# Kernel tuning notes

Hardware: AMD Instinct MI355X
Metric: run time of the kernel (lower is better)

Reference implementation:

```python
import jax, jax.numpy as jnp
import numpy as np

B, H, W, K = 4, 512, 512, 64
LAMBDA_SEP = 300.0
LAMBDA_MEAN = 300.0


def _huber(d):
    # torch.nn.functional.huber_loss elementwise, delta=1.0
    a = jnp.abs(d)
    return jnp.where(a < 1.0, 0.5 * a * a, a - 0.5)


def setup_inputs() -> dict:
    key = jax.random.key(0)
    k1, k2 = jax.random.split(key)
    prediction = jax.random.normal(k1, (B, 3, H, W), jnp.float32) * 2.0
    # integer instance labels in [0, K); force every instance to appear
    labels = jax.random.randint(k2, (B, H, W), 0, K)
    labels = labels.at[:, 0, :K].set(jnp.arange(K))
    # palette: instance k -> RGB (0, 0, k); id 0 is background (0,0,0)
    target = jnp.zeros((B, 3, H, W), jnp.float32).at[:, 2].set(labels.astype(jnp.float32))
    no_bg = jnp.ones((B,), bool)
    dist_weights = jnp.ones((K, K), jnp.float32)  # distances=None -> all weights 1.0
    palette_ids = jnp.arange(K, dtype=jnp.int32)  # r*65536 + g*256 + b per palette color
    return {"prediction": prediction, "target": target, "no_bg": no_bg,
            "dist_weights": dist_weights, "palette_ids": palette_ids}


def reference(prediction, target, no_bg, dist_weights, palette_ids):
    P = jnp.transpose(prediction, (0, 2, 3, 1)).astype(jnp.float32)  # [B,H,W,3]
    T = jnp.transpose(target, (0, 2, 3, 1))                          # [B,H,W,3]
    Kk = palette_ids.shape[0]
    h, w = P.shape[1], P.shape[2]
    # pixel instance id (exact for small int-valued floats)
    pid = T[..., 0] * 65536.0 + T[..., 1] * 256.0 + T[..., 2]        # [B,H,W]
    masks = (pid[..., None] == palette_ids.astype(pid.dtype)).astype(P.dtype)  # [B,H,W,K]
    counts = masks.sum((1, 2))                                       # [B,K]
    means = jnp.einsum('bhwk,bhwc->bkc', masks, P) / counts[..., None]  # [B,K,3]
    is_bg = palette_ids == 0                                          # [K]
    # bg instance is counted only when no_bg[b] is False
    counted = (~is_bg)[None, :] | (~no_bg)[:, None]                   # [B,K]
    cf = counted.astype(P.dtype)
    # --- intra-instance huber loss (toward instance mean; zeros for bg) ---
    means_z = jnp.where(is_bg[None, :, None], 0.0, means)             # bg target/mean = 0
    mean_pix = jnp.einsum('bhwk,bkc->bhwc', masks, means_z)           # per-pixel target
    hp = _huber(P - mean_pix).sum(-1)                                 # [B,H,W]
    intra_k = jnp.einsum('bhwk,bhw->bk', masks, hp) / (counts * 3.0)  # mean over pix*3
    intra = (intra_k * cf).sum(-1)                                    # [B]
    # --- inter-instance separation (non-bg instances only) ---
    P2 = (P * P).sum(-1)                                              # [B,H,W]
    M2 = (means * means).sum(-1)                                      # [B,K]
    d2 = P2[..., None] + M2[:, None, None, :] - 2.0 * jnp.einsum('bhwc,bkc->bhwk', P, means)
    sep = LAMBDA_SEP / (1.0 + d2)                                     # [B,H,W,K]
    w_pix = jnp.einsum('bhwj,kj->bhwk', masks, dist_weights)          # weight(k, inst(pixel))
    other = 1.0 - masks                                               # pixels not in k
    num = jnp.einsum('bhwk,bhwk,bhwk->bk', sep, w_pix, other)
    n_other = h * w - counts
    inter_k = num / n_other * (10.0 / jnp.sqrt(counts))
    inter = (inter_k * (~is_bg).astype(P.dtype)[None, :]).sum(-1)     # [B]
    # --- mean-level repulsion among counted instance means ---
    diff = means_z[:, :, None, :] - means_z[:, None, :, :]            # [B,K,K,3]
    sqd = (diff * diff).sum(-1)
    pen = dist_weights[None] * LAMBDA_MEAN / (sqd + 1.0)
    triu = jnp.triu(jnp.ones((Kk, Kk), P.dtype), k=1)
    pairmask = cf[:, :, None] * cf[:, None, :] * triu[None]
    npairs = pairmask.sum((1, 2))
    mean_sep = jnp.where(npairs > 0, (pen * pairmask).sum((1, 2)) / jnp.maximum(npairs, 1.0), 0.0)
    ct = jnp.maximum(cf.sum(-1), 1.0)
    loss_b = (intra + inter + mean_sep) / ct
    return jnp.mean(loss_b)
```

## Files before the change

kernel.cpp:

```cpp
#include <hip/hip_runtime.h>

#define KINST 64

typedef float v2f __attribute__((ext_vector_type(2)));

__device__ __forceinline__ int decode_k0(float t0, float t1, float t2,
                                         const int* pal_s) {
  int pid = (int)(fmaf(t0, 65536.f, fmaf(t1, 256.f, t2)) + 0.5f);
  if (pid >= 0 && pid < KINST && pal_s[pid] == pid) return pid;
  for (int j = 0; j < KINST; ++j)
    if (pal_s[j] == pid) return j;
  return KINST;
}

__global__ __launch_bounds__(256) void k_stats(const float* __restrict__ pred,
                                               const float* __restrict__ targ,
                                               const int* __restrict__ pal,
                                               float* __restrict__ partialS,
                                               unsigned char* __restrict__ k0c,
                                               float* __restrict__ out,
                                               int HW) {
  int b = blockIdx.y;
  __shared__ float ls[4][4][KINST];
  __shared__ int pal_s[KINST];
  if (blockIdx.x == 0 && blockIdx.y == 0 && threadIdx.x == 0) out[0] = 0.f;
  for (int i = threadIdx.x; i < 4 * 4 * KINST; i += blockDim.x)
    (&ls[0][0][0])[i] = 0.f;
  for (int i = threadIdx.x; i < KINST; i += blockDim.x) pal_s[i] = pal[i];
  __syncthreads();
  int w = threadIdx.x >> 6;
  const float* tb = targ + (size_t)b * 3 * HW;
  const float* pb = pred + (size_t)b * 3 * HW;
  unsigned char* kb = k0c ? k0c + (size_t)b * HW : nullptr;
  int nq = HW >> 2;
  const float4* tb4 = (const float4*)tb;
  const float4* pb4 = (const float4*)pb;
  for (int q = blockIdx.x * blockDim.x + threadIdx.x; q < nq;
       q += gridDim.x * blockDim.x) {
    float4 t0 = tb4[q], t1 = tb4[q + nq], t2 = tb4[q + 2 * nq];
    float4 p0 = pb4[q], p1 = pb4[q + nq], p2 = pb4[q + 2 * nq];
    int ka = decode_k0(t0.x, t1.x, t2.x, pal_s);
    int kc = decode_k0(t0.y, t1.y, t2.y, pal_s);
    int kd = decode_k0(t0.z, t1.z, t2.z, pal_s);
    int ke = decode_k0(t0.w, t1.w, t2.w, pal_s);
    if (ka < KINST) {
      atomicAdd(&ls[w][0][ka], p0.x); atomicAdd(&ls[w][1][ka], p1.x);
      atomicAdd(&ls[w][2][ka], p2.x); atomicAdd(&ls[w][3][ka], 1.f);
    }
    if (kc < KINST) {
      atomicAdd(&ls[w][0][kc], p0.y); atomicAdd(&ls[w][1][kc], p1.y);
      atomicAdd(&ls[w][2][kc], p2.y); atomicAdd(&ls[w][3][kc], 1.f);
    }
    if (kd < KINST) {
      atomicAdd(&ls[w][0][kd], p0.z); atomicAdd(&ls[w][1][kd], p1.z);
      atomicAdd(&ls[w][2][kd], p2.z); atomicAdd(&ls[w][3][kd], 1.f);
    }
    if (ke < KINST) {
      atomicAdd(&ls[w][0][ke], p0.w); atomicAdd(&ls[w][1][ke], p1.w);
      atomicAdd(&ls[w][2][ke], p2.w); atomicAdd(&ls[w][3][ke], 1.f);
    }
    if (kb) {
      uchar4 kk = make_uchar4((unsigned char)ka, (unsigned char)kc,
                              (unsigned char)kd, (unsigned char)ke);
      *(uchar4*)(kb + 4 * (size_t)q) = kk;
    }
  }
  for (int i = (nq << 2) + blockIdx.x * blockDim.x + threadIdx.x; i < HW;
       i += gridDim.x * blockDim.x) {
    int k0 = decode_k0(tb[i], tb[i + HW], tb[i + 2 * HW], pal_s);
    if (kb) kb[i] = (unsigned char)k0;
    if (k0 < KINST) {
      atomicAdd(&ls[w][0][k0], pb[i]); atomicAdd(&ls[w][1][k0], pb[i + HW]);
      atomicAdd(&ls[w][2][k0], pb[i + 2 * HW]); atomicAdd(&ls[w][3][k0], 1.f);
    }
  }
  __syncthreads();
  float* o = partialS + ((size_t)b * gridDim.x + blockIdx.x) * 256;
  int i = threadIdx.x;
  int c = i >> 6, k = i & 63;
  o[i] = ls[0][c][k] + ls[1][c][k] + ls[2][c][k] + ls[3][c][k];
}

__global__ __launch_bounds__(256) void k_reduce(const float* __restrict__ partialS,
                                                const float* __restrict__ dw,
                                                const int* __restrict__ pal,
                                                const unsigned char* __restrict__ nb_raw,
                                                int ndw, int nbs,
                                                float* __restrict__ sums,
                                                float4* __restrict__ A_g,
                                                float* __restrict__ W_g,
                                                float4* __restrict__ Z_g,
                                                float* __restrict__ cw_g,
                                                int* __restrict__ flagp,
                                                int B, int HW) {
  int b = blockIdx.x;
  int i = threadIdx.x;
  __shared__ float red[256];
  __shared__ float scale_sh[KINST];
  __shared__ int nu_sh;
  const float* src = partialS + (size_t)b * nbs * 256;
  float s0 = 0.f, s1 = 0.f, s2 = 0.f, s3 = 0.f;
  float s4 = 0.f, s5 = 0.f, s6 = 0.f, s7 = 0.f;
  int bx = 0;
  for (; bx + 8 <= nbs; bx += 8) {
    s0 += src[(size_t)(bx + 0) * 256 + i];
    s1 += src[(size_t)(bx + 1) * 256 + i];
    s2 += src[(size_t)(bx + 2) * 256 + i];
    s3 += src[(size_t)(bx + 3) * 256 + i];
    s4 += src[(size_t)(bx + 4) * 256 + i];
    s5 += src[(size_t)(bx + 5) * 256 + i];
    s6 += src[(size_t)(bx + 6) * 256 + i];
    s7 += src[(size_t)(bx + 7) * 256 + i];
  }
  for (; bx < nbs; ++bx) s0 += src[(size_t)bx * 256 + i];
  float acc = ((s0 + s1) + (s2 + s3)) + ((s4 + s5) + (s6 + s7));
  red[i] = acc;
  sums[((size_t)b * KINST + (i & 63)) * 4 + (i >> 6)] = acc;
  if (i == 0) nu_sh = 0;
  __syncthreads();
  {
    int per = (ndw + B - 1) / B;
    int lo = b * per, hi = min(lo + per, ndw);
    float d0 = dw[0];
    int nu = 0;
    for (int x = lo + i; x < hi; x += blockDim.x) nu |= (dw[x] != d0);
    if (nu) atomicOr(&nu_sh, 1);
  }
  __syncthreads();
  if (i < KINST) {
    float m0s = red[i], m1s = red[64 + i], m2s = red[128 + i], cnt = red[192 + i];
    float inv = cnt > 0.f ? 1.f / cnt : 0.f;
    float m0 = m0s * inv, m1 = m1s * inv, m2 = m2s * inv;
    bool isbg = (pal[i] == 0);
    bool nb = (nb_raw[b] != 0) || (nb_raw[4 * b] != 0);
    float cf = (!isbg || !nb) ? 1.f : 0.f;
    float sc = (!isbg && cnt > 0.f) ? 10.f / (((float)HW - cnt) * sqrtf(cnt)) : 0.f;
    A_g[b * 65 + i] = make_float4(-2.f * m0, -2.f * m1, -2.f * m2,
                                  m0 * m0 + m1 * m1 + m2 * m2 + 1.f);
    Z_g[b * 65 + i] = make_float4(isbg ? 0.f : m0, isbg ? 0.f : m1,
                                  isbg ? 0.f : m2,
                                  cnt > 0.f ? cf / (3.f * cnt) : 0.f);
    W_g[b * 65 + i] = 300.f * dw[0] * sc;
    scale_sh[i] = sc;
  }
  if (i == KINST) {
    A_g[b * 65 + KINST] = make_float4(0.f, 0.f, 0.f, 1.f);
    Z_g[b * 65 + KINST] = make_float4(0.f, 0.f, 0.f, 0.f);
    W_g[b * 65 + KINST] = 0.f;
  }
  __syncthreads();
  if (i == 0) flagp[b] = nu_sh;
  if (nu_sh) {
    float* ct = cw_g + (size_t)b * KINST * 65;
    for (int t2 = i; t2 < KINST * 65; t2 += blockDim.x) {
      int kk = t2 / 65, j = t2 - kk * 65;
      float v = 0.f;
      if (j < KINST && j != kk) v = 300.f * dw[kk * KINST + j] * scale_sh[kk];
      ct[t2] = v;
    }
  }
}

template <bool USE_CACHE>
__global__ __launch_bounds__(256) void k_pix(const float* __restrict__ pred,
                                             const float* __restrict__ targ,
                                             const unsigned char* __restrict__ k0c,
                                             const int* __restrict__ pal,
                                             const float4* __restrict__ A_g,
                                             const float* __restrict__ W_g,
                                             const float4* __restrict__ Z_g,
                                             const float* __restrict__ cw_g,
                                             const int* __restrict__ flagp,
                                             float* __restrict__ res_part,
                                             int HW, int B) {
  int b = blockIdx.y;
  __shared__ float4 A_s[KINST + 1];
  __shared__ float4 Z_s[KINST + 1];
  __shared__ float W_s[KINST + 1];
  __shared__ float cwN[KINST][KINST + 1];
  __shared__ int pal_s[KINST];
  __shared__ int nonuni_s;
  __shared__ float rA[4], rB[4];
  int t = threadIdx.x;
  if (t < KINST + 1) {
    A_s[t] = A_g[b * 65 + t];
    Z_s[t] = Z_g[b * 65 + t];
    W_s[t] = W_g[b * 65 + t];
  }
  if (!USE_CACHE && t < KINST) pal_s[t] = pal[t];
  if (t == 0) {
    int f = 0;
    for (int bb = 0; bb < B; ++bb) f |= flagp[bb];
    nonuni_s = f;
  }
  __syncthreads();
  bool nonuni = nonuni_s != 0;
  if (nonuni) {
    const float* cwb = cw_g + (size_t)b * KINST * 65;
    for (int i = t; i < KINST * 65; i += blockDim.x) (&cwN[0][0])[i] = cwb[i];
    __syncthreads();
  }
  const float* pb = pred + (size_t)b * 3 * HW;
  const float* tb = targ + (size_t)b * 3 * HW;
  const float4* pb4 = (const float4*)pb;
  const float4* tb4 = (const float4*)tb;
  int nq = HW >> 2;
  const uchar4* kb4 = USE_CACHE ? (const uchar4*)(k0c + (size_t)b * HW) : nullptr;
  float intra_l = 0.f, inter_l = 0.f;
  for (int q = blockIdx.x * blockDim.x + t; q < nq;
       q += gridDim.x * blockDim.x) {
    float4 P0 = pb4[q], P1 = pb4[q + nq], P2 = pb4[q + 2 * nq];
    int ka, kc, kd, ke;
    if (USE_CACHE) {
      uchar4 kk = kb4[q];
      ka = kk.x; kc = kk.y; kd = kk.z; ke = kk.w;
    } else {
      float4 T0 = tb4[q], T1 = tb4[q + nq], T2 = tb4[q + 2 * nq];
      ka = decode_k0(T0.x, T1.x, T2.x, pal_s);
      kc = decode_k0(T0.y, T1.y, T2.y, pal_s);
      kd = decode_k0(T0.z, T1.z, T2.z, pal_s);
      ke = decode_k0(T0.w, T1.w, T2.w, pal_s);
    }
    float ppa = fmaf(P0.x, P0.x, fmaf(P1.x, P1.x, P2.x * P2.x));
    float ppb = fmaf(P0.y, P0.y, fmaf(P1.y, P1.y, P2.y * P2.y));
    float ppc = fmaf(P0.z, P0.z, fmaf(P1.z, P1.z, P2.z * P2.z));
    float ppd = fmaf(P0.w, P0.w, fmaf(P1.w, P1.w, P2.w * P2.w));
    float aa = 0.f, ab = 0.f, ac = 0.f, ad = 0.f;
    if (!nonuni) {
      v2f pp01 = {ppa, ppb}, pp23 = {ppc, ppd};
      v2f P0a = {P0.x, P0.y}, P0b = {P0.z, P0.w};
      v2f P1a = {P1.x, P1.y}, P1b = {P1.z, P1.w};
      v2f P2a = {P2.x, P2.y}, P2b = {P2.z, P2.w};
      v2f acc01 = {0.f, 0.f}, acc23 = {0.f, 0.f};
      #pragma unroll 8
      for (int k = 0; k < KINST; ++k) {
        float4 a = A_s[k];
        float wv = W_s[k];
        v2f ax = {a.x, a.x}, ay = {a.y, a.y}, az = {a.z, a.z}, aw = {a.w, a.w};
        v2f wv2 = {wv, wv};
        v2f t01 = __builtin_elementwise_fma(P0a, ax, aw);
        t01 = __builtin_elementwise_fma(P1a, ay, t01);
        t01 = __builtin_elementwise_fma(P2a, az, t01);
        v2f arg01 = pp01 + t01;
        v2f t23 = __builtin_elementwise_fma(P0b, ax, aw);
        t23 = __builtin_elementwise_fma(P1b, ay, t23);
        t23 = __builtin_elementwise_fma(P2b, az, t23);
        v2f arg23 = pp23 + t23;
        v2f r01 = {__builtin_amdgcn_rcpf(arg01.x), __builtin_amdgcn_rcpf(arg01.y)};
        v2f r23 = {__builtin_amdgcn_rcpf(arg23.x), __builtin_amdgcn_rcpf(arg23.y)};
        acc01 = __builtin_elementwise_fma(r01, wv2, acc01);
        acc23 = __builtin_elementwise_fma(r23, wv2, acc23);
      }
      aa = acc01.x; ab = acc01.y; ac = acc23.x; ad = acc23.y;
      {
        float4 a = A_s[ka]; float wv = W_s[ka];
        float r = __builtin_amdgcn_rcpf(
            ppa + fmaf(P0.x, a.x, fmaf(P1.x, a.y, fmaf(P2.x, a.z, a.w))));
        aa = (ka < KINST) ? aa - wv * r : 0.f;
      }
      {
        float4 a = A_s[kc]; float wv = W_s[kc];
        float r = __builtin_amdgcn_rcpf(
            ppb + fmaf(P0.y, a.x, fmaf(P1.y, a.y, fmaf(P2.y, a.z, a.w))));
        ab = (kc < KINST) ? ab - wv * r : 0.f;
      }
      {
        float4 a = A_s[kd]; float wv = W_s[kd];
        float r = __builtin_amdgcn_rcpf(
            ppc + fmaf(P0.z, a.x, fmaf(P1.z, a.y, fmaf(P2.z, a.z, a.w))));
        ac = (kd < KINST) ? ac - wv * r : 0.f;
      }
      {
        float4 a = A_s[ke]; float wv = W_s[ke];
        float r = __builtin_amdgcn_rcpf(
            ppd + fmaf(P0.w, a.x, fmaf(P1.w, a.y, fmaf(P2.w, a.z, a.w))));
        ad = (ke < KINST) ? ad - wv * r : 0.f;
      }
    } else {
      #pragma unroll 4
      for (int k = 0; k < KINST; ++k) {
        float4 a = A_s[k];
        float ra = __builtin_amdgcn_rcpf(
            ppa + fmaf(P0.x, a.x, fmaf(P1.x, a.y, fmaf(P2.x, a.z, a.w))));
        float rb = __builtin_amdgcn_rcpf(
            ppb + fmaf(P0.y, a.x, fmaf(P1.y, a.y, fmaf(P2.y, a.z, a.w))));
        float rc = __builtin_amdgcn_rcpf(
            ppc + fmaf(P0.z, a.x, fmaf(P1.z, a.y, fmaf(P2.z, a.z, a.w))));
        float rd = __builtin_amdgcn_rcpf(
            ppd + fmaf(P0.w, a.x, fmaf(P1.w, a.y, fmaf(P2.w, a.z, a.w))));
        aa = fmaf(ra, cwN[k][ka], aa); ab = fmaf(rb, cwN[k][kc], ab);
        ac = fmaf(rc, cwN[k][kd], ac); ad = fmaf(rd, cwN[k][ke], ad);
      }
    }
    inter_l += (aa + ab) + (ac + ad);
    {
      float4 z = Z_s[ka];
      float q0 = fabsf(P0.x - z.x), q1 = fabsf(P1.x - z.y), q2 = fabsf(P2.x - z.z);
      float hp = (q0 < 1.f ? 0.5f * q0 * q0 : q0 - 0.5f) +
                 (q1 < 1.f ? 0.5f * q1 * q1 : q1 - 0.5f) +
                 (q2 < 1.f ? 0.5f * q2 * q2 : q2 - 0.5f);
      intra_l = fmaf(hp, z.w, intra_l);
    }
    {
      float4 z = Z_s[kc];
      float q0 = fabsf(P0.y - z.x), q1 = fabsf(P1.y - z.y), q2 = fabsf(P2.y - z.z);
      float hp = (q0 < 1.f ? 0.5f * q0 * q0 : q0 - 0.5f) +
                 (q1 < 1.f ? 0.5f * q1 * q1 : q1 - 0.5f) +
                 (q2 < 1.f ? 0.5f * q2 * q2 : q2 - 0.5f);
      intra_l = fmaf(hp, z.w, intra_l);
    }
    {
      float4 z = Z_s[kd];
      float q0 = fabsf(P0.z - z.x), q1 = fabsf(P1.z - z.y), q2 = fabsf(P2.z - z.z);
      float hp = (q0 < 1.f ? 0.5f * q0 * q0 : q0 - 0.5f) +
                 (q1 < 1.f ? 0.5f * q1 * q1 : q1 - 0.5f) +
                 (q2 < 1.f ? 0.5f * q2 * q2 : q2 - 0.5f);
      intra_l = fmaf(hp, z.w, intra_l);
    }
    {
      float4 z = Z_s[ke];
      float q0 = fabsf(P0.w - z.x), q1 = fabsf(P1.w - z.y), q2 = fabsf(P2.w - z.z);
      float hp = (q0 < 1.f ? 0.5f * q0 * q0 : q0 - 0.5f) +
                 (q1 < 1.f ? 0.5f * q1 * q1 : q1 - 0.5f) +
                 (q2 < 1.f ? 0.5f * q2 * q2 : q2 - 0.5f);
      intra_l = fmaf(hp, z.w, intra_l);
    }
  }
  for (int i = (nq << 2) + blockIdx.x * blockDim.x + t; i < HW;
       i += gridDim.x * blockDim.x) {
    float p0 = pb[i], p1 = pb[i + HW], p2 = pb[i + 2 * HW];
    int k0 = USE_CACHE ? (int)k0c[(size_t)b * HW + i]
                       : decode_k0(tb[i], tb[i + HW], tb[i + 2 * HW], pal_s);
    float pp = fmaf(p0, p0, fmaf(p1, p1, p2 * p2));
    float acc = 0.f;
    for (int k = 0; k < KINST; ++k) {
      float4 a = A_s[k];
      float r = __builtin_amdgcn_rcpf(
          pp + fmaf(p0, a.x, fmaf(p1, a.y, fmaf(p2, a.z, a.w))));
      float c = nonuni ? cwN[k][k0]
                       : ((k == k0 || k0 >= KINST) ? 0.f : W_s[k]);
      acc = fmaf(r, c, acc);
    }
    inter_l += acc;
    float4 z = Z_s[k0];
    float q0 = fabsf(p0 - z.x), q1 = fabsf(p1 - z.y), q2 = fabsf(p2 - z.z);
    float hp = (q0 < 1.f ? 0.5f * q0 * q0 : q0 - 0.5f) +
               (q1 < 1.f ? 0.5f * q1 * q1 : q1 - 0.5f) +
               (q2 < 1.f ? 0.5f * q2 * q2 : q2 - 0.5f);
    intra_l = fmaf(hp, z.w, intra_l);
  }
  for (int o = 32; o > 0; o >>= 1) {
    intra_l += __shfl_down(intra_l, o, 64);
    inter_l += __shfl_down(inter_l, o, 64);
  }
  int wid = t >> 6;
  if ((t & 63) == 0) { rA[wid] = intra_l; rB[wid] = inter_l; }
  __syncthreads();
  if (t == 0) {
    float a = 0.f, c = 0.f;
    for (int i = 0; i < 4; ++i) { a += rA[i]; c += rB[i]; }
    float* rp = res_part + ((size_t)b * gridDim.x + blockIdx.x) * 2;
    rp[0] = a; rp[1] = c;
  }
}

__global__ __launch_bounds__(256) void k_final(const float* __restrict__ sums,
                                               const int* __restrict__ pal,
                                               const unsigned char* __restrict__ nb_raw,
                                               const float* __restrict__ dw,
                                               const float* __restrict__ res_part,
                                               int ngx,
                                               float* __restrict__ out,
                                               int B, int HW) {
  int b = blockIdx.x;
  __shared__ float4 zf[KINST];
  __shared__ float rA[4], rB[4], rC[4], rD[4], rE[4];
  int t = threadIdx.x;
  if (t < KINST) {
    float4 s = ((const float4*)sums)[b * KINST + t];
    float cnt = s.w;
    float inv = cnt > 0.f ? 1.f / cnt : 0.f;
    bool isbg = (pal[t] == 0);
    bool nb = (nb_raw[b] != 0) || (nb_raw[4 * b] != 0);
    float cf = (!isbg || !nb) ? 1.f : 0.f;
    zf[t] = make_float4(isbg ? 0.f : s.x * inv, isbg ? 0.f : s.y * inv,
                        isbg ? 0.f : s.z * inv, cf);
  }
  __syncthreads();
  float psum = 0.f, pcnt = 0.f, cfs = 0.f, ra = 0.f, rc = 0.f;
  for (int idx = t; idx < KINST * KINST; idx += blockDim.x) {
    int j = idx >> 6, k = idx & 63;
    if (j < k) {
      float4 a = zf[j], c4 = zf[k];
      float m = a.w * c4.w;
      float d0 = a.x - c4.x, d1 = a.y - c4.y, d2 = a.z - c4.z;
      float sqd = d0 * d0 + d1 * d1 + d2 * d2;
      psum += dw[j * KINST + k] * 300.f / (sqd + 1.f) * m;
      pcnt += m;
    }
  }
  if (t < KINST) cfs = zf[t].w;
  for (int bx = t; bx < ngx; bx += blockDim.x) {
    const float* rp = res_part + ((size_t)b * ngx + bx) * 2;
    ra += rp[0]; rc += rp[1];
  }
  for (int o = 32; o > 0; o >>= 1) {
    psum += __shfl_down(psum, o, 64);
    pcnt += __shfl_down(pcnt, o, 64);
    cfs += __shfl_down(cfs, o, 64);
    ra += __shfl_down(ra, o, 64);
    rc += __shfl_down(rc, o, 64);
  }
  int wid = t >> 6;
  if ((t & 63) == 0) {
    rA[wid] = psum; rB[wid] = pcnt; rC[wid] = cfs; rD[wid] = ra; rE[wid] = rc;
  }
  __syncthreads();
  if (t == 0) {
    float ps = 0.f, pc = 0.f, cs = 0.f, sa = 0.f, sc2 = 0.f;
    for (int i = 0; i < 4; ++i) {
      ps += rA[i]; pc += rB[i]; cs += rC[i]; sa += rD[i]; sc2 += rE[i];
    }
    float mean_sep = pc > 0.f ? ps / fmaxf(pc, 1.f) : 0.f;
    float ct = fmaxf(cs, 1.f);
    atomicAdd(out, ((sa + sc2 + mean_sep) / ct) / (float)B);
  }
}

extern "C" void kernel_launch(void* const* d_in, const int* in_sizes, int n_in,
                              void* d_out, int out_size, void* d_ws, size_t ws_size,
                              hipStream_t stream) {
  const float* pred = (const float*)d_in[0];
  const float* targ = (const float*)d_in[1];
  const unsigned char* nb = (const unsigned char*)d_in[2];
  const float* dw = (const float*)d_in[3];
  const int* pal = (const int*)d_in[4];
  int B = in_sizes[2];
  int ndw = in_sizes[3];
  int HW = in_sizes[0] / (3 * B);
  const int GX = 256;

  auto floats_needed = [&](int nbs) -> size_t {
    return (size_t)B * nbs * 256 + (size_t)B * 256 + (size_t)B * GX * 2 + B +
           (size_t)B * 65 * 4 + (size_t)B * 65 + (size_t)B * 65 * 4 +
           (size_t)B * KINST * 65;
  };
  int nbs = 128;
  bool use_cache = true;
  if (ws_size < floats_needed(128) * 4 + (size_t)B * HW) {
    if (ws_size >= floats_needed(32) * 4 + (size_t)B * HW) nbs = 32;
    else { nbs = 32; use_cache = false; }
  }
  float* partialS = (float*)d_ws;
  float* sums = partialS + (size_t)B * nbs * 256;
  float* res_part = sums + (size_t)B * 256;
  int* flagp = (int*)(res_part + (size_t)B * GX * 2);
  float4* A_g = (float4*)(flagp + B);
  float* W_g = (float*)(A_g + (size_t)B * 65);
  float4* Z_g = (float4*)(W_g + (size_t)B * 65);
  float* cw_g = (float*)(Z_g + (size_t)B * 65);
  unsigned char* k0c = use_cache ? (unsigned char*)(cw_g + (size_t)B * KINST * 65)
                                 : nullptr;

  k_stats<<<dim3(nbs, B), 256, 0, stream>>>(pred, targ, pal, partialS, k0c,
                                            (float*)d_out, HW);
  k_reduce<<<B, 256, 0, stream>>>(partialS, dw, pal, nb, ndw, nbs, sums, A_g,
                                  W_g, Z_g, cw_g, flagp, B, HW);
  if (use_cache)
    k_pix<true><<<dim3(GX, B), 256, 0, stream>>>(pred, targ, k0c, pal, A_g, W_g,
                                                 Z_g, cw_g, flagp, res_part, HW, B);
  else
    k_pix<false><<<dim3(GX, B), 256, 0, stream>>>(pred, targ, k0c, pal, A_g, W_g,
                                                  Z_g, cw_g, flagp, res_part, HW, B);
  k_final<<<B, 256, 0, stream>>>(sums, pal, nb, dw, res_part, GX,
                                 (float*)d_out, B, HW);
}
```

Before: 55.00 us.

## Fold per-batch stats reduction into pixel and final kernels, drop k_reduce launch

Removes the separate k_reduce kernel. Each k_pix block now reduces the per-block partial sums itself and builds the per-instance mean, scale and weight tables directly in shared memory, and k_final redoes the same reduction. This saves one launch and its global round trip. In exchange, every one of the 256×B pixel blocks redundantly reads nbs×256 partials and scans the full distance-weight matrix, and the stats grid is cut from 128 to 64 blocks per batch so that redundant reduction stays small.

Result: faster. 53.43 us (-2.8%).

```diff
diff --git a/kernel.cpp b/kernel.cpp
--- a/kernel.cpp
+++ b/kernel.cpp
@@ -81,24 +81,8 @@
   o[i] = ls[0][c][k] + ls[1][c][k] + ls[2][c][k] + ls[3][c][k];
 }
 
-__global__ __launch_bounds__(256) void k_reduce(const float* __restrict__ partialS,
-                                                const float* __restrict__ dw,
-                                                const int* __restrict__ pal,
-                                                const unsigned char* __restrict__ nb_raw,
-                                                int ndw, int nbs,
-                                                float* __restrict__ sums,
-                                                float4* __restrict__ A_g,
-                                                float* __restrict__ W_g,
-                                                float4* __restrict__ Z_g,
-                                                float* __restrict__ cw_g,
-                                                int* __restrict__ flagp,
-                                                int B, int HW) {
-  int b = blockIdx.x;
-  int i = threadIdx.x;
-  __shared__ float red[256];
-  __shared__ float scale_sh[KINST];
-  __shared__ int nu_sh;
-  const float* src = partialS + (size_t)b * nbs * 256;
+__device__ __forceinline__ float reduce_partials(const float* __restrict__ src,
+                                                 int nbs, int i) {
   float s0 = 0.f, s1 = 0.f, s2 = 0.f, s3 = 0.f;
   float s4 = 0.f, s5 = 0.f, s6 = 0.f, s7 = 0.f;
   int bx = 0;
@@ -113,52 +97,7 @@
     s7 += src[(size_t)(bx + 7) * 256 + i];
   }
   for (; bx < nbs; ++bx) s0 += src[(size_t)bx * 256 + i];
-  float acc = ((s0 + s1) + (s2 + s3)) + ((s4 + s5) + (s6 + s7));
-  red[i] = acc;
-  sums[((size_t)b * KINST + (i & 63)) * 4 + (i >> 6)] = acc;
-  if (i == 0) nu_sh = 0;
-  __syncthreads();
-  {
-    int per = (ndw + B - 1) / B;
-    int lo = b * per, hi = min(lo + per, ndw);
-    float d0 = dw[0];
-    int nu = 0;
-    for (int x = lo + i; x < hi; x += blockDim.x) nu |= (dw[x] != d0);
-    if (nu) atomicOr(&nu_sh, 1);
-  }
-  __syncthreads();
-  if (i < KINST) {
-    float m0s = red[i], m1s = red[64 + i], m2s = red[128 + i], cnt = red[192 + i];
-    float inv = cnt > 0.f ? 1.f / cnt : 0.f;
-    float m0 = m0s * inv, m1 = m1s * inv, m2 = m2s * inv;
-    bool isbg = (pal[i] == 0);
-    bool nb = (nb_raw[b] != 0) || (nb_raw[4 * b] != 0);
-    float cf = (!isbg || !nb) ? 1.f : 0.f;
-    float sc = (!isbg && cnt > 0.f) ? 10.f / (((float)HW - cnt) * sqrtf(cnt)) : 0.f;
-    A_g[b * 65 + i] = make_float4(-2.f * m0, -2.f * m1, -2.f * m2,
-                                  m0 * m0 + m1 * m1 + m2 * m2 + 1.f);
-    Z_g[b * 65 + i] = make_float4(isbg ? 0.f : m0, isbg ? 0.f : m1,
-                                  isbg ? 0.f : m2,
-                                  cnt > 0.f ? cf / (3.f * cnt) : 0.f);
-    W_g[b * 65 + i] = 300.f * dw[0] * sc;
-    scale_sh[i] = sc;
-  }
-  if (i == KINST) {
-    A_g[b * 65 + KINST] = make_float4(0.f, 0.f, 0.f, 1.f);
-    Z_g[b * 65 + KINST] = make_float4(0.f, 0.f, 0.f, 0.f);
-    W_g[b * 65 + KINST] = 0.f;
-  }
-  __syncthreads();
-  if (i == 0) flagp[b] = nu_sh;
-  if (nu_sh) {
-    float* ct = cw_g + (size_t)b * KINST * 65;
-    for (int t2 = i; t2 < KINST * 65; t2 += blockDim.x) {
-      int kk = t2 / 65, j = t2 - kk * 65;
-      float v = 0.f;
-      if (j < KINST && j != kk) v = 300.f * dw[kk * KINST + j] * scale_sh[kk];
-      ct[t2] = v;
-    }
-  }
+  return ((s0 + s1) + (s2 + s3)) + ((s4 + s5) + (s6 + s7));
 }
 
 template <bool USE_CACHE>
@@ -166,38 +105,64 @@
                                              const float* __restrict__ targ,
                                              const unsigned char* __restrict__ k0c,
                                              const int* __restrict__ pal,
-                                             const float4* __restrict__ A_g,
-                                             const float* __restrict__ W_g,
-                                             const float4* __restrict__ Z_g,
-                                             const float* __restrict__ cw_g,
-                                             const int* __restrict__ flagp,
+                                             const float* __restrict__ partialS,
+                                             const unsigned char* __restrict__ nb_raw,
+                                             const float* __restrict__ dw,
+                                             int ndw, int nbs,
                                              float* __restrict__ res_part,
                                              int HW, int B) {
   int b = blockIdx.y;
+  __shared__ float red[256];
+  __shared__ float scale_sh[KINST];
   __shared__ float4 A_s[KINST + 1];
   __shared__ float4 Z_s[KINST + 1];
   __shared__ float W_s[KINST + 1];
   __shared__ float cwN[KINST][KINST + 1];
   __shared__ int pal_s[KINST];
-  __shared__ int nonuni_s;
+  __shared__ int nu_sh;
   __shared__ float rA[4], rB[4];
   int t = threadIdx.x;
-  if (t < KINST + 1) {
-    A_s[t] = A_g[b * 65 + t];
-    Z_s[t] = Z_g[b * 65 + t];
-    W_s[t] = W_g[b * 65 + t];
-  }
+  red[t] = reduce_partials(partialS + (size_t)b * nbs * 256, nbs, t);
+  if (t == 0) nu_sh = 0;
   if (!USE_CACHE && t < KINST) pal_s[t] = pal[t];
-  if (t == 0) {
-    int f = 0;
-    for (int bb = 0; bb < B; ++bb) f |= flagp[bb];
-    nonuni_s = f;
-  }
-  __syncthreads();
-  bool nonuni = nonuni_s != 0;
+  __syncthreads();
+  {
+    float d0 = dw[0];
+    int nu = 0;
+    for (int x = t; x < ndw; x += blockDim.x) nu |= (dw[x] != d0);
+    if (nu) atomicOr(&nu_sh, 1);
+  }
+  __syncthreads();
+  if (t < KINST) {
+    float m0s = red[t], m1s = red[64 + t], m2s = red[128 + t],
+          cnt = red[192 + t];
+    float inv = cnt > 0.f ? 1.f / cnt : 0.f;
+    float m0 = m0s * inv, m1 = m1s * inv, m2 = m2s * inv;
+    bool isbg = (pal[t] == 0);
+    bool nb = (nb_raw[b] != 0) || (nb_raw[4 * b] != 0);
+    float cf = (!isbg || !nb) ? 1.f : 0.f;
+    float sc = (!isbg && cnt > 0.f) ? 10.f / (((float)HW - cnt) * sqrtf(cnt)) : 0.f;
+    A_s[t] = make_float4(-2.f * m0, -2.f * m1, -2.f * m2,
+                         m0 * m0 + m1 * m1 + m2 * m2 + 1.f);
+    Z_s[t] = make_float4(isbg ? 0.f : m0, isbg ? 0.f : m1, isbg ? 0.f : m2,
+                         cnt > 0.f ? cf / (3.f * cnt) : 0.f);
+    W_s[t] = 300.f * dw[0] * sc;
+    scale_sh[t] = sc;
+  }
+  if (t == KINST) {
+    A_s[KINST] = make_float4(0.f, 0.f, 0.f, 1.f);
+    Z_s[KINST] = make_float4(0.f, 0.f, 0.f, 0.f);
+    W_s[KINST] = 0.f;
+  }
+  __syncthreads();
+  bool nonuni = nu_sh != 0;
   if (nonuni) {
-    const float* cwb = cw_g + (size_t)b * KINST * 65;
-    for (int i = t; i < KINST * 65; i += blockDim.x) (&cwN[0][0])[i] = cwb[i];
+    for (int i = t; i < KINST * (KINST + 1); i += blockDim.x) {
+      int kk = i / (KINST + 1), j = i - kk * (KINST + 1);
+      float v = 0.f;
+      if (j < KINST && j != kk) v = 300.f * dw[kk * KINST + j] * scale_sh[kk];
+      (&cwN[0][0])[i] = v;
+    }
     __syncthreads();
   }
   const float* pb = pred + (size_t)b * 3 * HW;
@@ -364,27 +329,29 @@
   }
 }
 
-__global__ __launch_bounds__(256) void k_final(const float* __restrict__ sums,
+__global__ __launch_bounds__(256) void k_final(const float* __restrict__ partialS,
                                                const int* __restrict__ pal,
                                                const unsigned char* __restrict__ nb_raw,
                                                const float* __restrict__ dw,
                                                const float* __restrict__ res_part,
-                                               int ngx,
-                                               float* __restrict__ out,
-                                               int B, int HW) {
+                                               int nbs, int ngx,
+                                               float* __restrict__ out, int B) {
   int b = blockIdx.x;
+  int t = threadIdx.x;
+  __shared__ float red[256];
   __shared__ float4 zf[KINST];
   __shared__ float rA[4], rB[4], rC[4], rD[4], rE[4];
-  int t = threadIdx.x;
+  red[t] = reduce_partials(partialS + (size_t)b * nbs * 256, nbs, t);
+  __syncthreads();
   if (t < KINST) {
-    float4 s = ((const float4*)sums)[b * KINST + t];
-    float cnt = s.w;
+    float m0s = red[t], m1s = red[64 + t], m2s = red[128 + t],
+          cnt = red[192 + t];
     float inv = cnt > 0.f ? 1.f / cnt : 0.f;
     bool isbg = (pal[t] == 0);
     bool nb = (nb_raw[b] != 0) || (nb_raw[4 * b] != 0);
     float cf = (!isbg || !nb) ? 1.f : 0.f;
-    zf[t] = make_float4(isbg ? 0.f : s.x * inv, isbg ? 0.f : s.y * inv,
-                        isbg ? 0.f : s.z * inv, cf);
+    zf[t] = make_float4(isbg ? 0.f : m0s * inv, isbg ? 0.f : m1s * inv,
+                        isbg ? 0.f : m2s * inv, cf);
   }
   __syncthreads();
   float psum = 0.f, pcnt = 0.f, cfs = 0.f, ra = 0.f, rc = 0.f;
@@ -441,37 +408,29 @@
   const int GX = 256;
 
   auto floats_needed = [&](int nbs) -> size_t {
-    return (size_t)B * nbs * 256 + (size_t)B * 256 + (size_t)B * GX * 2 + B +
-           (size_t)B * 65 * 4 + (size_t)B * 65 + (size_t)B * 65 * 4 +
-           (size_t)B * KINST * 65;
+    return (size_t)B * nbs * 256 + (size_t)B * GX * 2;
   };
-  int nbs = 128;
+  int nbs = 64;
   bool use_cache = true;
-  if (ws_size < floats_needed(128) * 4 + (size_t)B * HW) {
+  if (ws_size < floats_needed(64) * 4 + (size_t)B * HW) {
     if (ws_size >= floats_needed(32) * 4 + (size_t)B * HW) nbs = 32;
     else { nbs = 32; use_cache = false; }
   }
   float* partialS = (float*)d_ws;
-  float* sums = partialS + (size_t)B * nbs * 256;
-  float* res_part = sums + (size_t)B * 256;
-  int* flagp = (int*)(res_part + (size_t)B * GX * 2);
-  float4* A_g = (float4*)(flagp + B);
-  float* W_g = (float*)(A_g + (size_t)B * 65);
-  float4* Z_g = (float4*)(W_g + (size_t)B * 65);
-  float* cw_g = (float*)(Z_g + (size_t)B * 65);
-  unsigned char* k0c = use_cache ? (unsigned char*)(cw_g + (size_t)B * KINST * 65)
+  float* res_part = partialS + (size_t)B * nbs * 256;
+  unsigned char* k0c = use_cache ? (unsigned char*)(res_part + (size_t)B * GX * 2)
                                  : nullptr;
 
   k_stats<<<dim3(nbs, B), 256, 0, stream>>>(pred, targ, pal, partialS, k0c,
                                             (float*)d_out, HW);
-  k_reduce<<<B, 256, 0, stream>>>(partialS, dw, pal, nb, ndw, nbs, sums, A_g,
-                                  W_g, Z_g, cw_g, flagp, B, HW);
   if (use_cache)
-    k_pix<true><<<dim3(GX, B), 256, 0, stream>>>(pred, targ, k0c, pal, A_g, W_g,
-                                                 Z_g, cw_g, flagp, res_part, HW, B);
+    k_pix<true><<<dim3(GX, B), 256, 0, stream>>>(pred, targ, k0c, pal, partialS,
+                                                 nb, dw, ndw, nbs, res_part,
+                                                 HW, B);
   else
-    k_pix<false><<<dim3(GX, B), 256, 0, stream>>>(pred, targ, k0c, pal, A_g, W_g,
-                                                  Z_g, cw_g, flagp, res_part, HW, B);
-  k_final<<<B, 256, 0, stream>>>(sums, pal, nb, dw, res_part, GX,
-                                 (float*)d_out, B, HW);
-}
+    k_pix<false><<<dim3(GX, B), 256, 0, stream>>>(pred, targ, k0c, pal, partialS,
+                                                  nb, dw, ndw, nbs, res_part,
+                                                  HW, B);
+  k_final<<<B, 256, 0, stream>>>(partialS, pal, nb, dw, res_part, nbs, GX,
+                                 (float*)d_out, B);
+}
```
